# Kernel optimization log

Hardware: AMD Instinct MI355X
Metric: run time of the kernel (lower is better)

The kernel has to match this reference:

```python
import jax, jax.numpy as jnp
import numpy as np

B, S, DM = 4, 2048, 1024
H, D, R = 16, 64, 8

def setup_inputs() -> dict:
    key = jax.random.key(0)
    ks = jax.random.split(key, 32)
    def rn(k, shape, scale=0.02):
        return jax.random.normal(k, shape, dtype=jnp.float32) * scale
    inp = {
        'queries': jax.random.normal(ks[0], (B, S, DM), dtype=jnp.float32),
        'keys':    jax.random.normal(ks[1], (B, S, DM), dtype=jnp.float32),
        'values':  jax.random.normal(ks[2], (B, S, DM), dtype=jnp.float32),
        # base projections, stored [in, out]
        'Wq_w': rn(ks[3], (DM, H * D)), 'Wq_b': jnp.zeros((H * D,), jnp.float32),
        'Wk_w': rn(ks[4], (DM, H * D)), 'Wk_b': jnp.zeros((H * D,), jnp.float32),
        'Wv_w': rn(ks[5], (DM, H * D)), 'Wv_b': jnp.zeros((H * D,), jnp.float32),
        # LoRA adapters (A: in->rank, B: rank->out), Linear layers so both have biases
        'Aq_w': rn(ks[6], (DM, R)), 'Aq_b': jnp.zeros((R,), jnp.float32),
        'Bq_w': rn(ks[7], (R, H * D)), 'Bq_b': jnp.zeros((H * D,), jnp.float32),
        'Ak_w': rn(ks[8], (DM, R)), 'Ak_b': jnp.zeros((R,), jnp.float32),
        'Bk_w': rn(ks[9], (R, H * D)), 'Bk_b': jnp.zeros((H * D,), jnp.float32),
        'Av_w': rn(ks[10], (DM, R)), 'Av_b': jnp.zeros((R,), jnp.float32),
        'Bv_w': rn(ks[11], (R, H * D)), 'Bv_b': jnp.zeros((H * D,), jnp.float32),
        # output merge
        'Wo_w': rn(ks[12], (H * D, DM)), 'Wo_b': jnp.zeros((DM,), jnp.float32),
    }
    return inp


def _attn(queries, keys, values, Wq_w, Wq_b, Wk_w, Wk_b, Wv_w, Wv_b,
          Aq_w, Aq_b, Bq_w, Bq_b, Ak_w, Ak_b, Bk_w, Bk_b, Av_w, Av_b, Bv_w, Bv_b,
          Wo_w, Wo_b):
    b, s, _ = queries.shape
    # QKV projections fused with LoRA low-rank additions
    q = queries @ Wq_w + Wq_b + ((queries @ Aq_w + Aq_b) @ Bq_w + Bq_b)
    k = keys    @ Wk_w + Wk_b + ((keys    @ Ak_w + Ak_b) @ Bk_w + Bk_b)
    # NOTE: source applies the V LoRA adapter to `keys` (self.Av(keys)) - replicated
    v = values  @ Wv_w + Wv_b + ((keys    @ Av_w + Av_b) @ Bv_w + Bv_b)
    q = q.reshape(b, s, H, D).transpose(0, 2, 1, 3)  # [B,H,S,D]
    k = k.reshape(b, s, H, D).transpose(0, 2, 1, 3)
    v = v.reshape(b, s, H, D).transpose(0, 2, 1, 3)
    att = jnp.einsum('bhqd,bhkd->bhqk', q, k)        # [B,H,Sq,Sk]
    causal = jnp.tril(jnp.ones((s, s), dtype=bool))
    att = jnp.where(causal, att, -jnp.inf)
    # NOTE: source softmaxes over dim=2 (query axis) and scales AFTER softmax
    att = jax.nn.softmax(att, axis=2) / jnp.sqrt(jnp.asarray(D, att.dtype))
    out = jnp.einsum('bhqk,bhkd->bhqd', att, v)      # [B,H,S,D]
    out = out.transpose(0, 2, 1, 3).reshape(b, s, H * D)
    return out @ Wo_w + Wo_b


def reference(queries, keys, values, Wq_w, Wq_b, Wk_w, Wk_b, Wv_w, Wv_b,
              Aq_w, Aq_b, Bq_w, Bq_b, Ak_w, Ak_b, Bk_w, Bk_b, Av_w, Av_b, Bv_w, Bv_b,
              Wo_w, Wo_b):
    return _attn(queries, keys, values, Wq_w, Wq_b, Wk_w, Wk_b, Wv_w, Wv_b,
                 Aq_w, Aq_b, Bq_w, Bq_b, Ak_w, Ak_b, Bk_w, Bk_b, Av_w, Av_b, Bv_w, Bv_b,
                 Wo_w, Wo_b)
```

## Files before the change

### kernel.cpp

```cpp
#include <hip/hip_runtime.h>
#include <math.h>
#include <stdint.h>

typedef __bf16 bf16;
typedef __bf16 bf16x8 __attribute__((ext_vector_type(8)));
typedef __bf16 bf16x4 __attribute__((ext_vector_type(4)));
typedef float  floatx4 __attribute__((ext_vector_type(4)));

#define MFMA16(a, b, c) __builtin_amdgcn_mfma_f32_16x16x32_bf16(a, b, c, 0, 0, 0)
#define EXP2(x) __builtin_amdgcn_exp2f(x)

static constexpr int S  = 2048;
static constexpr int DM = 1024;
static constexpr int Dh = 64;
#define NEGBIG (-1e30f)
#define LOG2E  1.44269504088896340736f

__device__ __forceinline__ void gload16(const void* g, void* l) {
  __builtin_amdgcn_global_load_lds(
      (const __attribute__((address_space(1))) void*)(uintptr_t)g,
      (__attribute__((address_space(3))) void*)(uintptr_t)l,
      16, 0, 0);
}

__device__ __forceinline__ int swz(int row, int g) {
  return row * 64 + ((g ^ (row & 7)) << 3);
}

__global__ __launch_bounds__(256) void prep_convert(
    const float* __restrict__ q, const float* __restrict__ k,
    const float* __restrict__ v, bf16* __restrict__ X)
{
  int s = blockIdx.x;
  int c = threadIdx.x * 4;
  size_t src = (size_t)s * DM + c;
  float4 qv = *(const float4*)(q + src);
  float4 vv = *(const float4*)(v + src);
  float4 kv = *(const float4*)(k + src);
  size_t dst = (size_t)s * (3 * DM);
  bf16x4 t;
  t[0] = (bf16)qv.x; t[1] = (bf16)qv.y; t[2] = (bf16)qv.z; t[3] = (bf16)qv.w;
  *(bf16x4*)(X + dst + c) = t;
  t[0] = (bf16)vv.x; t[1] = (bf16)vv.y; t[2] = (bf16)vv.z; t[3] = (bf16)vv.w;
  *(bf16x4*)(X + dst + DM + c) = t;
  t[0] = (bf16)kv.x; t[1] = (bf16)kv.y; t[2] = (bf16)kv.z; t[3] = (bf16)kv.w;
  *(bf16x4*)(X + dst + 2 * DM + c) = t;
}

__global__ __launch_bounds__(256) void fold_weights(
    const float* __restrict__ Wq, const float* __restrict__ Aq, const float* __restrict__ Bq,
    const float* __restrict__ Wk, const float* __restrict__ Ak, const float* __restrict__ Bk,
    const float* __restrict__ Wv, const float* __restrict__ Av, const float* __restrict__ Bv,
    const float* __restrict__ Wo,
    bf16* __restrict__ WqT, bf16* __restrict__ WkT,
    bf16* __restrict__ WvT, bf16* __restrict__ WoT)
{
  __shared__ float tile[32][33];
  const int tx = threadIdx.x, ty = threadIdx.y;
  const int n0 = blockIdx.x * 32, k0 = blockIdx.y * 32;
  for (int mi = 0; mi < 5; ++mi) {
    #pragma unroll
    for (int i = 0; i < 4; ++i) {
      int k = k0 + ty + i * 8, n = n0 + tx;
      float val = 0.f;
      if (mi == 0) {
        val = Wq[(size_t)k * DM + n];
        #pragma unroll
        for (int r = 0; r < 8; ++r) val += Aq[k * 8 + r] * Bq[(size_t)r * DM + n];
      } else if (mi == 1) {
        val = Wk[(size_t)k * DM + n];
        #pragma unroll
        for (int r = 0; r < 8; ++r) val += Ak[k * 8 + r] * Bk[(size_t)r * DM + n];
      } else if (mi == 2) {
        val = Wv[(size_t)k * DM + n];
      } else if (mi == 3) {
        #pragma unroll
        for (int r = 0; r < 8; ++r) val += Av[k * 8 + r] * Bv[(size_t)r * DM + n];
      } else {
        val = Wo[(size_t)k * DM + n];
      }
      tile[ty + i * 8][tx] = val;
    }
    __syncthreads();
    #pragma unroll
    for (int i = 0; i < 4; ++i) {
      int n = n0 + ty + i * 8, k = k0 + tx;
      float val = tile[tx][ty + i * 8];
      if (mi == 0)      WqT[(size_t)n * DM + k] = (bf16)val;
      else if (mi == 1) WkT[(size_t)n * DM + k] = (bf16)val;
      else if (mi == 2) WvT[(size_t)n * 2048 + k] = (bf16)val;
      else if (mi == 3) WvT[(size_t)n * 2048 + 1024 + k] = (bf16)val;
      else              WoT[(size_t)n * DM + k] = (bf16)val;
    }
    __syncthreads();
  }
}

__global__ __launch_bounds__(256) void fold_bias(
    const float* __restrict__ Wqb, const float* __restrict__ Aqb,
    const float* __restrict__ BqW, const float* __restrict__ Bqb,
    const float* __restrict__ Wkb, const float* __restrict__ Akb,
    const float* __restrict__ BkW, const float* __restrict__ Bkb,
    const float* __restrict__ Wvb, const float* __restrict__ Avb,
    const float* __restrict__ BvW, const float* __restrict__ Bvb,
    const float* __restrict__ Wob,
    float* __restrict__ bq, float* __restrict__ bk,
    float* __restrict__ bv, float* __restrict__ bo)
{
  int n = blockIdx.x * 256 + threadIdx.x;
  float aq = Wqb[n] + Bqb[n];
  float ak = Wkb[n] + Bkb[n];
  float av = Wvb[n] + Bvb[n];
  #pragma unroll
  for (int r = 0; r < 8; ++r) {
    aq += Aqb[r] * BqW[(size_t)r * DM + n];
    ak += Akb[r] * BkW[(size_t)r * DM + n];
    av += Avb[r] * BvW[(size_t)r * DM + n];
  }
  bq[n] = aq; bk[n] = ak; bv[n] = av; bo[n] = Wob[n];
}

__global__ __launch_bounds__(256) void gemm_bf16(
    const bf16* __restrict__ A, int lda,
    const bf16* __restrict__ BT, int ldb,
    const float* __restrict__ bias,
    int M, int N, int K, float oscale,
    float* __restrict__ outF, bf16* __restrict__ outB, int mode)
{
  __shared__ bf16 sA[128 * 32];
  __shared__ bf16 sB[128 * 32];
  const int tid = threadIdx.x;
  const int bm0 = blockIdx.y * 128, bn0 = blockIdx.x * 128;
  const int w = tid >> 6, lane = tid & 63, lrow = lane & 15, quad = lane >> 4;
  const int wm = (w >> 1) * 64, wn = (w & 1) * 64;

  const int srow = lane >> 2;
  const int scol = (lane & 3) * 8;
  const bf16* Ag0 = A  + (size_t)(bm0 + w * 32 + srow) * lda + scol;
  const bf16* Ag1 = A  + (size_t)(bm0 + w * 32 + 16 + srow) * lda + scol;
  const bf16* Bg0 = BT + (size_t)(bn0 + w * 32 + srow) * ldb + scol;
  const bf16* Bg1 = BT + (size_t)(bn0 + w * 32 + 16 + srow) * ldb + scol;
  bf16* sA0 = &sA[(w * 32) * 32];
  bf16* sA1 = &sA[(w * 32 + 16) * 32];
  bf16* sB0 = &sB[(w * 32) * 32];
  bf16* sB1 = &sB[(w * 32 + 16) * 32];

  floatx4 zero = {0.f, 0.f, 0.f, 0.f};
  floatx4 acc[4][4];
  #pragma unroll
  for (int i = 0; i < 4; ++i)
    #pragma unroll
    for (int j = 0; j < 4; ++j) acc[i][j] = zero;

  for (int kt = 0; kt < K; kt += 32) {
    __syncthreads();
    gload16(Ag0 + kt, sA0);
    gload16(Ag1 + kt, sA1);
    gload16(Bg0 + kt, sB0);
    gload16(Bg1 + kt, sB1);
    __syncthreads();
    bf16x8 aF[4], bF[4];
    #pragma unroll
    for (int i = 0; i < 4; ++i)
      aF[i] = *(const bf16x8*)&sA[(wm + i * 16 + lrow) * 32 + quad * 8];
    #pragma unroll
    for (int j = 0; j < 4; ++j)
      bF[j] = *(const bf16x8*)&sB[(wn + j * 16 + lrow) * 32 + quad * 8];
    #pragma unroll
    for (int i = 0; i < 4; ++i)
      #pragma unroll
      for (int j = 0; j < 4; ++j)
        acc[i][j] = MFMA16(aF[i], bF[j], acc[i][j]);
  }

  if (mode == 3) {
    #pragma unroll
    for (int i = 0; i < 4; ++i) {
      #pragma unroll
      for (int r = 0; r < 4; ++r) {
        int gm = bm0 + wm + i * 16 + quad * 4 + r;
        float bvr = bias[gm];
        int h = gm >> 6, d = gm & 63;
        #pragma unroll
        for (int j = 0; j < 4; ++j) {
          int gn = bn0 + wn + j * 16 + lrow;
          int b = gn >> 11, s = gn & 2047;
          outB[((size_t)(b * 16 + h) * 64 + d) * 2048 + s] =
              (bf16)(acc[i][j][r] + bvr);
        }
      }
    }
    return;
  }

  float bvs[4];
  #pragma unroll
  for (int j = 0; j < 4; ++j) bvs[j] = bias[bn0 + wn + j * 16 + lrow];

  #pragma unroll
  for (int i = 0; i < 4; ++i) {
    #pragma unroll
    for (int j = 0; j < 4; ++j) {
      #pragma unroll
      for (int r = 0; r < 4; ++r) {
        int gm = bm0 + wm + i * 16 + quad * 4 + r;
        int gn = bn0 + wn + j * 16 + lrow;
        float v = (acc[i][j][r] + bvs[j]) * oscale;
        if (mode == 0) {
          outF[(size_t)gm * N + gn] = v;
        } else {
          int b = gm >> 11, s = gm & 2047, h = gn >> 6, d = gn & 63;
          outB[((size_t)(b * 16 + h) * 2048 + s) * 64 + d] = (bf16)v;
        }
      }
    }
  }
}

__global__ __launch_bounds__(256) void attn_pass1(
    const bf16* __restrict__ Qb, const bf16* __restrict__ Kb,
    float* __restrict__ statC)
{
  const int bh = blockIdx.y;
  const int x = blockIdx.x;
  const int q0a = x * 64, q0b = (31 - x) * 64;
  const int tid = threadIdx.x;
  const int w = tid >> 6, lane = tid & 63, lrow = lane & 15, quad = lane >> 4;
  const bf16* Qh = Qb + (size_t)bh * S * Dh;
  const bf16* Kh = Kb + (size_t)bh * S * Dh;

  int cbase[8];
  #pragma unroll
  for (int cf = 0; cf < 8; ++cf)
    cbase[cf] = (cf < 4) ? (q0a + cf * 16) : (q0b + (cf - 4) * 16);

  bf16x8 kf[8][2];
  #pragma unroll
  for (int cf = 0; cf < 8; ++cf) {
    const bf16* kp = Kh + (size_t)(cbase[cf] + lrow) * Dh + quad * 8;
    kf[cf][0] = *(const bf16x8*)kp;
    kf[cf][1] = *(const bf16x8*)(kp + 32);
  }

  float rm[8], rs[8];
  #pragma unroll
  for (int cf = 0; cf < 8; ++cf) { rm[cf] = NEGBIG; rs[cf] = 0.f; }

  const int qs = q0a + w * 16;
  const bf16* qp0 = Qh + (size_t)(qs + lrow) * Dh + quad * 8;
  bf16x8 a0 = *(const bf16x8*)qp0, a1 = *(const bf16x8*)(qp0 + 32);

  for (int q0 = qs; q0 < S; q0 += 64) {
    bf16x8 n0 = a0, n1 = a1;
    if (q0 + 64 < S) {
      const bf16* np = Qh + (size_t)(q0 + 64 + lrow) * Dh + quad * 8;
      n0 = *(const bf16x8*)np; n1 = *(const bf16x8*)(np + 32);
    }
    #pragma unroll
    for (int cf = 0; cf < 8; ++cf) {
      const int c0f = cbase[cf];
      if (c0f > q0 + 15) continue;
      floatx4 sacc = {0.f, 0.f, 0.f, 0.f};
      sacc = MFMA16(a0, kf[cf][0], sacc);
      sacc = MFMA16(a1, kf[cf][1], sacc);
      float v0 = sacc[0], v1 = sacc[1], v2 = sacc[2], v3 = sacc[3];
      if (q0 < c0f + 15) {
        int c = c0f + lrow, qb = q0 + quad * 4;
        v0 = (qb + 0 >= c) ? v0 : NEGBIG;
        v1 = (qb + 1 >= c) ? v1 : NEGBIG;
        v2 = (qb + 2 >= c) ? v2 : NEGBIG;
        v3 = (qb + 3 >= c) ? v3 : NEGBIG;
      }
      float mt = fmaxf(fmaxf(v0, v1), fmaxf(v2, v3));
      float nm = fmaxf(rm[cf], mt);
      rs[cf] = rs[cf] * EXP2(rm[cf] - nm)
             + EXP2(v0 - nm) + EXP2(v1 - nm)
             + EXP2(v2 - nm) + EXP2(v3 - nm);
      rm[cf] = nm;
    }
    a0 = n0; a1 = n1;
  }

  #pragma unroll
  for (int cf = 0; cf < 8; ++cf) {
    #pragma unroll
    for (int off = 16; off < 64; off <<= 1) {
      float om = __shfl_xor(rm[cf], off, 64);
      float os = __shfl_xor(rs[cf], off, 64);
      float nm = fmaxf(rm[cf], om);
      rs[cf] = rs[cf] * EXP2(rm[cf] - nm) + os * EXP2(om - nm);
      rm[cf] = nm;
    }
  }

  __shared__ float smm[4][128];
  __shared__ float sms[4][128];
  if (quad == 0) {
    #pragma unroll
    for (int cf = 0; cf < 8; ++cf) {
      smm[w][cf * 16 + lrow] = rm[cf];
      sms[w][cf * 16 + lrow] = rs[cf];
    }
  }
  __syncthreads();
  if (tid < 128) {
    float m = smm[0][tid], sum = sms[0][tid];
    #pragma unroll
    for (int ww = 1; ww < 4; ++ww) {
      float om = smm[ww][tid], os = sms[ww][tid];
      float nm = fmaxf(m, om);
      sum = sum * EXP2(m - nm) + os * EXP2(om - nm);
      m = nm;
    }
    int col = (tid < 64) ? (q0a + tid) : (q0b + tid - 64);
    statC[(size_t)bh * S + col] = m + 3.0f + __log2f(sum);
  }
}

__global__ __launch_bounds__(256) void attn_pass2(
    const bf16* __restrict__ Qb, const bf16* __restrict__ Kb,
    const bf16* __restrict__ Vt, const float* __restrict__ statC,
    bf16* __restrict__ AttOut)
{
  const int bh = blockIdx.y;
  const int x = blockIdx.x;
  const int q0a = x * 64, q0b = (31 - x) * 64;
  const int tid = threadIdx.x;
  const int w = tid >> 6, lane = tid & 63, lrow = lane & 15, quad = lane >> 4;
  const bf16* Qh = Qb + (size_t)bh * S * Dh;
  const bf16* Kh = Kb + (size_t)bh * S * Dh;
  const bf16* Vh = Vt + (size_t)bh * Dh * S;
  const float* sth = statC + (size_t)bh * S;

  __shared__ bf16 sK[64 * 64];
  __shared__ bf16 sV[64 * 64];
  __shared__ bf16 pbuf[4][32 * 64];

  const int r0m[2] = { q0a + w * 16, q0b + w * 16 };
  bf16x8 qf[2][2];
  #pragma unroll
  for (int mi = 0; mi < 2; ++mi) {
    const bf16* qp = Qh + (size_t)(r0m[mi] + lrow) * Dh + quad * 8;
    qf[mi][0] = *(const bf16x8*)qp;
    qf[mi][1] = *(const bf16x8*)(qp + 32);
  }

  floatx4 zero = {0.f, 0.f, 0.f, 0.f};
  floatx4 accO[2][4];
  #pragma unroll
  for (int mi = 0; mi < 2; ++mi)
    #pragma unroll
    for (int nf = 0; nf < 4; ++nf) accO[mi][nf] = zero;

  const int sr = tid >> 3;
  const int g  = tid & 7;
  const int nT = 32 - x;
  bf16* const pw = &pbuf[w][0];

  bf16x8 kg0 = *(const bf16x8*)(Kh + (size_t)sr * Dh + g * 8);
  bf16x8 kg1 = *(const bf16x8*)(Kh + (size_t)(sr + 32) * Dh + g * 8);
  bf16x8 vg0 = *(const bf16x8*)(Vh + (size_t)sr * S + g * 8);
  bf16x8 vg1 = *(const bf16x8*)(Vh + (size_t)(sr + 32) * S + g * 8);

  for (int kt = 0; kt < nT; ++kt) {
    const int kc = kt * 64;
    __syncthreads();
    *(bf16x8*)&sK[swz(sr, g)]      = kg0;
    *(bf16x8*)&sK[swz(sr + 32, g)] = kg1;
    *(bf16x8*)&sV[swz(sr, g)]      = vg0;
    *(bf16x8*)&sV[swz(sr + 32, g)] = vg1;
    float4 c4[4];
    #pragma unroll
    for (int cf = 0; cf < 4; ++cf)
      c4[cf] = *(const float4*)&sth[kc + cf * 16 + quad * 4];
    __syncthreads();
    if (kt + 1 < nT) {
      const int kn = kc + 64;
      kg0 = *(const bf16x8*)(Kh + (size_t)(kn + sr) * Dh + g * 8);
      kg1 = *(const bf16x8*)(Kh + (size_t)(kn + sr + 32) * Dh + g * 8);
      vg0 = *(const bf16x8*)(Vh + (size_t)sr * S + kn + g * 8);
      vg1 = *(const bf16x8*)(Vh + (size_t)(sr + 32) * S + kn + g * 8);
    }

    bool actH[2][2];
    #pragma unroll
    for (int mi = 0; mi < 2; ++mi) {
      actH[mi][0] = kc      <= r0m[mi] + 15;
      actH[mi][1] = kc + 32 <= r0m[mi] + 15;
    }

    #pragma unroll
    for (int cf = 0; cf < 4; ++cf) {
      const int hh = cf >> 1;
      if (!actH[0][hh] && !actH[1][hh]) continue;
      const int c0f = kc + cf * 16;
      const int cl = cf * 16;
      bf16x8 kf0 = *(const bf16x8*)&sK[swz(cl + lrow, quad)];
      bf16x8 kf1 = *(const bf16x8*)&sK[swz(cl + lrow, 4 + quad)];
      const float* cc = &c4[cf].x;
      const int crb = c0f + quad * 4;
      #pragma unroll
      for (int mi = 0; mi < 2; ++mi) {
        if (!actH[mi][hh]) continue;
        const int r0 = r0m[mi];
        const int gq = cf * 2 + (quad >> 1);
        const int poff = (mi * 16 + lrow) * 64 +
                         ((gq ^ (lrow & 7)) << 3) + (quad & 1) * 4;
        bf16x4 pk;
        if (c0f > r0 + 15) {
          pk[0] = pk[1] = pk[2] = pk[3] = (bf16)0.f;
        } else {
          floatx4 sacc = zero;
          sacc = MFMA16(kf0, qf[mi][0], sacc);
          sacc = MFMA16(kf1, qf[mi][1], sacc);
          const bool fullf = (c0f + 15 <= r0);
          const int qlane = r0 + lrow;
          #pragma unroll
          for (int r = 0; r < 4; ++r) {
            float p = EXP2(sacc[r] - cc[r]);
            if (!fullf) p = (crb + r <= qlane) ? p : 0.f;
            pk[r] = (bf16)p;
          }
        }
        *(bf16x4*)(pw + poff) = pk;
      }
    }

    #pragma unroll
    for (int hh = 0; hh < 2; ++hh) {
      if (!actH[0][hh] && !actH[1][hh]) continue;
      bf16x8 vf[4];
      #pragma unroll
      for (int nf = 0; nf < 4; ++nf)
        vf[nf] = *(const bf16x8*)&sV[swz(nf * 16 + lrow, hh * 4 + quad)];
      #pragma unroll
      for (int mi = 0; mi < 2; ++mi) {
        if (!actH[mi][hh]) continue;
        bf16x8 pf = *(const bf16x8*)(pw + swz(mi * 16 + lrow, hh * 4 + quad));
        #pragma unroll
        for (int nf = 0; nf < 4; ++nf)
          accO[mi][nf] = MFMA16(pf, vf[nf], accO[mi][nf]);
      }
    }
  }

  const int b = bh >> 4, h = bh & 15;
  #pragma unroll
  for (int mi = 0; mi < 2; ++mi) {
    #pragma unroll
    for (int nf = 0; nf < 4; ++nf) {
      #pragma unroll
      for (int r = 0; r < 4; ++r) {
        int qq = r0m[mi] + quad * 4 + r;
        int d = nf * 16 + lrow;
        AttOut[((size_t)(b * S + qq)) * DM + h * 64 + d] = (bf16)accO[mi][nf][r];
      }
    }
  }
}

extern "C" void kernel_launch(void* const* d_in, const int* in_sizes, int n_in,
                              void* d_out, int out_size, void* d_ws, size_t ws_size,
                              hipStream_t stream) {
  (void)in_sizes; (void)n_in; (void)out_size; (void)ws_size;
  const float* queries = (const float*)d_in[0];
  const float* keys    = (const float*)d_in[1];
  const float* values  = (const float*)d_in[2];
  const float* Wq_w = (const float*)d_in[3];  const float* Wq_b = (const float*)d_in[4];
  const float* Wk_w = (const float*)d_in[5];  const float* Wk_b = (const float*)d_in[6];
  const float* Wv_w = (const float*)d_in[7];  const float* Wv_b = (const float*)d_in[8];
  const float* Aq_w = (const float*)d_in[9];  const float* Aq_b = (const float*)d_in[10];
  const float* Bq_w = (const float*)d_in[11]; const float* Bq_b = (const float*)d_in[12];
  const float* Ak_w = (const float*)d_in[13]; const float* Ak_b = (const float*)d_in[14];
  const float* Bk_w = (const float*)d_in[15]; const float* Bk_b = (const float*)d_in[16];
  const float* Av_w = (const float*)d_in[17]; const float* Av_b = (const float*)d_in[18];
  const float* Bv_w = (const float*)d_in[19]; const float* Bv_b = (const float*)d_in[20];
  const float* Wo_w = (const float*)d_in[21]; const float* Wo_b = (const float*)d_in[22];
  float* out = (float*)d_out;

  char* ws = (char*)d_ws;
  size_t off = 0;
  auto alloc = [&](size_t bytes) -> void* {
    void* p = ws + off;
    off += (bytes + 255) & ~(size_t)255;
    return p;
  };
  bf16*  X_all  = (bf16*)alloc((size_t)8192 * 3072 * 2);
  bf16*  Qb     = (bf16*)alloc((size_t)64 * 2048 * 64 * 2);
  bf16*  Kb     = (bf16*)alloc((size_t)64 * 2048 * 64 * 2);
  bf16*  Vt     = (bf16*)alloc((size_t)64 * 64 * 2048 * 2);
  bf16*  AttOut = (bf16*)alloc((size_t)8192 * 1024 * 2);
  bf16*  WqT    = (bf16*)alloc((size_t)1024 * 1024 * 2);
  bf16*  WkT    = (bf16*)alloc((size_t)1024 * 1024 * 2);
  bf16*  WvT    = (bf16*)alloc((size_t)1024 * 2048 * 2);
  bf16*  WoT    = (bf16*)alloc((size_t)1024 * 1024 * 2);
  float* bq     = (float*)alloc(1024 * 4);
  float* bk     = (float*)alloc(1024 * 4);
  float* bv     = (float*)alloc(1024 * 4);
  float* bo     = (float*)alloc(1024 * 4);
  float* statC  = (float*)alloc((size_t)64 * 2048 * 4);

  prep_convert<<<8192, 256, 0, stream>>>(queries, keys, values, X_all);
  fold_weights<<<dim3(32, 32), dim3(32, 8), 0, stream>>>(
      Wq_w, Aq_w, Bq_w, Wk_w, Ak_w, Bk_w, Wv_w, Av_w, Bv_w, Wo_w,
      WqT, WkT, WvT, WoT);
  fold_bias<<<4, 256, 0, stream>>>(
      Wq_b, Aq_b, Bq_w, Bq_b, Wk_b, Ak_b, Bk_w, Bk_b,
      Wv_b, Av_b, Bv_w, Bv_b, Wo_b, bq, bk, bv, bo);

  gemm_bf16<<<dim3(8, 64), 256, 0, stream>>>(X_all,        3072, WqT, 1024, bq, 8192, 1024, 1024, LOG2E, nullptr, Qb, 1);
  gemm_bf16<<<dim3(8, 64), 256, 0, stream>>>(X_all + 2048, 3072, WkT, 1024, bk, 8192, 1024, 1024, 1.0f,  nullptr, Kb, 1);
  gemm_bf16<<<dim3(64, 8), 256, 0, stream>>>(WvT, 2048, X_all + 1024, 3072, bv, 1024, 8192, 2048, 1.0f, nullptr, Vt, 3);

  attn_pass1<<<dim3(16, 64), 256, 0, stream>>>(Qb, Kb, statC);
  attn_pass2<<<dim3(16, 64), 256, 0, stream>>>(Qb, Kb, Vt, statC, AttOut);

  gemm_bf16<<<dim3(8, 64), 256, 0, stream>>>(AttOut, 1024, WoT, 1024, bo, 8192, 1024, 1024, 1.0f, out, nullptr, 0);
}
```

Measured before the change: 471.5 us.

## Double-buffer swizzled GEMM tiles and split attention pass2 across eight waves

The bf16 GEMM moves to 512 threads per block with 8 waves, each owning a 32x64 sub-tile. It double-buffers the A/B LDS tiles with a single barrier per k-step, prefetching the next tile while the current one feeds the MFMAs, and adds an XOR swizzle on LDS columns to reduce bank conflicts. attn_pass2 also moves to 512 threads, so each wave handles one 16-row query strip instead of two, which halves per-wave accumulators and P buffers. The aims are to hide global-load latency and raise occupancy. The cost is more barrier participants per block and reliance on the async LDS loads having completed at the barrier.

```diff
diff --git a/kernel.cpp b/kernel.cpp
--- a/kernel.cpp
+++ b/kernel.cpp
@@ -120,54 +120,63 @@
   bq[n] = aq; bk[n] = ak; bv[n] = av; bo[n] = Wob[n];
 }
 
-__global__ __launch_bounds__(256) void gemm_bf16(
+__global__ __launch_bounds__(512, 4) void gemm_bf16(
     const bf16* __restrict__ A, int lda,
     const bf16* __restrict__ BT, int ldb,
     const float* __restrict__ bias,
     int M, int N, int K, float oscale,
     float* __restrict__ outF, bf16* __restrict__ outB, int mode)
 {
-  __shared__ bf16 sA[128 * 32];
-  __shared__ bf16 sB[128 * 32];
+  __shared__ bf16 sA[2][128 * 32];
+  __shared__ bf16 sB[2][128 * 32];
   const int tid = threadIdx.x;
   const int bm0 = blockIdx.y * 128, bn0 = blockIdx.x * 128;
   const int w = tid >> 6, lane = tid & 63, lrow = lane & 15, quad = lane >> 4;
-  const int wm = (w >> 1) * 64, wn = (w & 1) * 64;
-
-  const int srow = lane >> 2;
-  const int scol = (lane & 3) * 8;
-  const bf16* Ag0 = A  + (size_t)(bm0 + w * 32 + srow) * lda + scol;
-  const bf16* Ag1 = A  + (size_t)(bm0 + w * 32 + 16 + srow) * lda + scol;
-  const bf16* Bg0 = BT + (size_t)(bn0 + w * 32 + srow) * ldb + scol;
-  const bf16* Bg1 = BT + (size_t)(bn0 + w * 32 + 16 + srow) * ldb + scol;
-  bf16* sA0 = &sA[(w * 32) * 32];
-  bf16* sA1 = &sA[(w * 32 + 16) * 32];
-  bf16* sB0 = &sB[(w * 32) * 32];
-  bf16* sB1 = &sB[(w * 32 + 16) * 32];
+  const int wm = (w >> 1) * 32, wn = (w & 1) * 64;
+
+  const int srow = tid >> 2;
+  const int sg   = (tid & 3) ^ ((srow >> 1) & 3);
+  const bf16* Ag = A  + (size_t)(bm0 + srow) * lda + sg * 8;
+  const bf16* Bg = BT + (size_t)(bn0 + srow) * ldb + sg * 8;
+  const int wb = w * 512;
+
+  int aoff[2], boff[4];
+  #pragma unroll
+  for (int i = 0; i < 2; ++i) {
+    int r = wm + i * 16 + lrow;
+    aoff[i] = r * 32 + ((quad ^ ((r >> 1) & 3)) << 3);
+  }
+  #pragma unroll
+  for (int j = 0; j < 4; ++j) {
+    int r = wn + j * 16 + lrow;
+    boff[j] = r * 32 + ((quad ^ ((r >> 1) & 3)) << 3);
+  }
 
   floatx4 zero = {0.f, 0.f, 0.f, 0.f};
-  floatx4 acc[4][4];
-  #pragma unroll
-  for (int i = 0; i < 4; ++i)
+  floatx4 acc[2][4];
+  #pragma unroll
+  for (int i = 0; i < 2; ++i)
     #pragma unroll
     for (int j = 0; j < 4; ++j) acc[i][j] = zero;
 
-  for (int kt = 0; kt < K; kt += 32) {
+  const int nk = K >> 5;
+  gload16(Ag, &sA[0][wb]);
+  gload16(Bg, &sB[0][wb]);
+
+  for (int t = 0; t < nk; ++t) {
+    const int cur = t & 1;
     __syncthreads();
-    gload16(Ag0 + kt, sA0);
-    gload16(Ag1 + kt, sA1);
-    gload16(Bg0 + kt, sB0);
-    gload16(Bg1 + kt, sB1);
-    __syncthreads();
-    bf16x8 aF[4], bF[4];
-    #pragma unroll
-    for (int i = 0; i < 4; ++i)
-      aF[i] = *(const bf16x8*)&sA[(wm + i * 16 + lrow) * 32 + quad * 8];
-    #pragma unroll
-    for (int j = 0; j < 4; ++j)
-      bF[j] = *(const bf16x8*)&sB[(wn + j * 16 + lrow) * 32 + quad * 8];
-    #pragma unroll
-    for (int i = 0; i < 4; ++i)
+    if (t + 1 < nk) {
+      gload16(Ag + (size_t)(t + 1) * 32, &sA[cur ^ 1][wb]);
+      gload16(Bg + (size_t)(t + 1) * 32, &sB[cur ^ 1][wb]);
+    }
+    bf16x8 aF[2], bF[4];
+    #pragma unroll
+    for (int i = 0; i < 2; ++i) aF[i] = *(const bf16x8*)&sA[cur][aoff[i]];
+    #pragma unroll
+    for (int j = 0; j < 4; ++j) bF[j] = *(const bf16x8*)&sB[cur][boff[j]];
+    #pragma unroll
+    for (int i = 0; i < 2; ++i)
       #pragma unroll
       for (int j = 0; j < 4; ++j)
         acc[i][j] = MFMA16(aF[i], bF[j], acc[i][j]);
@@ -175,7 +184,7 @@
 
   if (mode == 3) {
     #pragma unroll
-    for (int i = 0; i < 4; ++i) {
+    for (int i = 0; i < 2; ++i) {
       #pragma unroll
       for (int r = 0; r < 4; ++r) {
         int gm = bm0 + wm + i * 16 + quad * 4 + r;
@@ -198,7 +207,7 @@
   for (int j = 0; j < 4; ++j) bvs[j] = bias[bn0 + wn + j * 16 + lrow];
 
   #pragma unroll
-  for (int i = 0; i < 4; ++i) {
+  for (int i = 0; i < 2; ++i) {
     #pragma unroll
     for (int j = 0; j < 4; ++j) {
       #pragma unroll
@@ -317,7 +326,7 @@
   }
 }
 
-__global__ __launch_bounds__(256) void attn_pass2(
+__global__ __launch_bounds__(512, 8) void attn_pass2(
     const bf16* __restrict__ Qb, const bf16* __restrict__ Kb,
     const bf16* __restrict__ Vt, const float* __restrict__ statC,
     bf16* __restrict__ AttOut)
@@ -327,6 +336,8 @@
   const int q0a = x * 64, q0b = (31 - x) * 64;
   const int tid = threadIdx.x;
   const int w = tid >> 6, lane = tid & 63, lrow = lane & 15, quad = lane >> 4;
+  const int mi = w >> 2;
+  const int r0 = (mi ? q0b : q0a) + (w & 3) * 16;
   const bf16* Qh = Qb + (size_t)bh * S * Dh;
   const bf16* Kh = Kb + (size_t)bh * S * Dh;
   const bf16* Vh = Vt + (size_t)bh * Dh * S;
@@ -334,127 +345,98 @@
 
   __shared__ bf16 sK[64 * 64];
   __shared__ bf16 sV[64 * 64];
-  __shared__ bf16 pbuf[4][32 * 64];
-
-  const int r0m[2] = { q0a + w * 16, q0b + w * 16 };
-  bf16x8 qf[2][2];
-  #pragma unroll
-  for (int mi = 0; mi < 2; ++mi) {
-    const bf16* qp = Qh + (size_t)(r0m[mi] + lrow) * Dh + quad * 8;
-    qf[mi][0] = *(const bf16x8*)qp;
-    qf[mi][1] = *(const bf16x8*)(qp + 32);
-  }
+  __shared__ bf16 pbuf[8][16 * 64];
+
+  const bf16* qp = Qh + (size_t)(r0 + lrow) * Dh + quad * 8;
+  bf16x8 qf0 = *(const bf16x8*)qp;
+  bf16x8 qf1 = *(const bf16x8*)(qp + 32);
 
   floatx4 zero = {0.f, 0.f, 0.f, 0.f};
-  floatx4 accO[2][4];
-  #pragma unroll
-  for (int mi = 0; mi < 2; ++mi)
-    #pragma unroll
-    for (int nf = 0; nf < 4; ++nf) accO[mi][nf] = zero;
+  floatx4 accO[4];
+  #pragma unroll
+  for (int nf = 0; nf < 4; ++nf) accO[nf] = zero;
 
   const int sr = tid >> 3;
   const int g  = tid & 7;
   const int nT = 32 - x;
   bf16* const pw = &pbuf[w][0];
 
-  bf16x8 kg0 = *(const bf16x8*)(Kh + (size_t)sr * Dh + g * 8);
-  bf16x8 kg1 = *(const bf16x8*)(Kh + (size_t)(sr + 32) * Dh + g * 8);
-  bf16x8 vg0 = *(const bf16x8*)(Vh + (size_t)sr * S + g * 8);
-  bf16x8 vg1 = *(const bf16x8*)(Vh + (size_t)(sr + 32) * S + g * 8);
+  bf16x8 kg = *(const bf16x8*)(Kh + (size_t)sr * Dh + g * 8);
+  bf16x8 vg = *(const bf16x8*)(Vh + (size_t)sr * S + g * 8);
 
   for (int kt = 0; kt < nT; ++kt) {
     const int kc = kt * 64;
     __syncthreads();
-    *(bf16x8*)&sK[swz(sr, g)]      = kg0;
-    *(bf16x8*)&sK[swz(sr + 32, g)] = kg1;
-    *(bf16x8*)&sV[swz(sr, g)]      = vg0;
-    *(bf16x8*)&sV[swz(sr + 32, g)] = vg1;
+    *(bf16x8*)&sK[swz(sr, g)] = kg;
+    *(bf16x8*)&sV[swz(sr, g)] = vg;
+    __syncthreads();
     float4 c4[4];
     #pragma unroll
     for (int cf = 0; cf < 4; ++cf)
       c4[cf] = *(const float4*)&sth[kc + cf * 16 + quad * 4];
-    __syncthreads();
     if (kt + 1 < nT) {
       const int kn = kc + 64;
-      kg0 = *(const bf16x8*)(Kh + (size_t)(kn + sr) * Dh + g * 8);
-      kg1 = *(const bf16x8*)(Kh + (size_t)(kn + sr + 32) * Dh + g * 8);
-      vg0 = *(const bf16x8*)(Vh + (size_t)sr * S + kn + g * 8);
-      vg1 = *(const bf16x8*)(Vh + (size_t)(sr + 32) * S + kn + g * 8);
-    }
-
-    bool actH[2][2];
-    #pragma unroll
-    for (int mi = 0; mi < 2; ++mi) {
-      actH[mi][0] = kc      <= r0m[mi] + 15;
-      actH[mi][1] = kc + 32 <= r0m[mi] + 15;
-    }
+      kg = *(const bf16x8*)(Kh + (size_t)(kn + sr) * Dh + g * 8);
+      vg = *(const bf16x8*)(Vh + (size_t)sr * S + kn + g * 8);
+    }
+
+    const bool act0 = kc      <= r0 + 15;
+    const bool act1 = kc + 32 <= r0 + 15;
 
     #pragma unroll
     for (int cf = 0; cf < 4; ++cf) {
-      const int hh = cf >> 1;
-      if (!actH[0][hh] && !actH[1][hh]) continue;
+      const bool acth = (cf >> 1) ? act1 : act0;
+      if (!acth) continue;
       const int c0f = kc + cf * 16;
       const int cl = cf * 16;
-      bf16x8 kf0 = *(const bf16x8*)&sK[swz(cl + lrow, quad)];
-      bf16x8 kf1 = *(const bf16x8*)&sK[swz(cl + lrow, 4 + quad)];
-      const float* cc = &c4[cf].x;
-      const int crb = c0f + quad * 4;
-      #pragma unroll
-      for (int mi = 0; mi < 2; ++mi) {
-        if (!actH[mi][hh]) continue;
-        const int r0 = r0m[mi];
-        const int gq = cf * 2 + (quad >> 1);
-        const int poff = (mi * 16 + lrow) * 64 +
-                         ((gq ^ (lrow & 7)) << 3) + (quad & 1) * 4;
-        bf16x4 pk;
-        if (c0f > r0 + 15) {
-          pk[0] = pk[1] = pk[2] = pk[3] = (bf16)0.f;
-        } else {
-          floatx4 sacc = zero;
-          sacc = MFMA16(kf0, qf[mi][0], sacc);
-          sacc = MFMA16(kf1, qf[mi][1], sacc);
-          const bool fullf = (c0f + 15 <= r0);
-          const int qlane = r0 + lrow;
-          #pragma unroll
-          for (int r = 0; r < 4; ++r) {
-            float p = EXP2(sacc[r] - cc[r]);
-            if (!fullf) p = (crb + r <= qlane) ? p : 0.f;
-            pk[r] = (bf16)p;
-          }
+      const int gq = cf * 2 + (quad >> 1);
+      const int poff = lrow * 64 + ((gq ^ (lrow & 7)) << 3) + (quad & 1) * 4;
+      bf16x4 pk;
+      if (c0f > r0 + 15) {
+        pk[0] = pk[1] = pk[2] = pk[3] = (bf16)0.f;
+      } else {
+        bf16x8 kf0 = *(const bf16x8*)&sK[swz(cl + lrow, quad)];
+        bf16x8 kf1 = *(const bf16x8*)&sK[swz(cl + lrow, 4 + quad)];
+        floatx4 sacc = zero;
+        sacc = MFMA16(kf0, qf0, sacc);
+        sacc = MFMA16(kf1, qf1, sacc);
+        const float* cc = &c4[cf].x;
+        const int crb = c0f + quad * 4;
+        const bool fullf = (c0f + 15 <= r0);
+        const int qlane = r0 + lrow;
+        #pragma unroll
+        for (int r = 0; r < 4; ++r) {
+          float p = EXP2(sacc[r] - cc[r]);
+          if (!fullf) p = (crb + r <= qlane) ? p : 0.f;
+          pk[r] = (bf16)p;
         }
-        *(bf16x4*)(pw + poff) = pk;
       }
+      *(bf16x4*)(pw + poff) = pk;
     }
 
     #pragma unroll
     for (int hh = 0; hh < 2; ++hh) {
-      if (!actH[0][hh] && !actH[1][hh]) continue;
+      const bool acth = hh ? act1 : act0;
+      if (!acth) continue;
       bf16x8 vf[4];
       #pragma unroll
       for (int nf = 0; nf < 4; ++nf)
         vf[nf] = *(const bf16x8*)&sV[swz(nf * 16 + lrow, hh * 4 + quad)];
+      bf16x8 pf = *(const bf16x8*)(pw + swz(lrow, hh * 4 + quad));
       #pragma unroll
-      for (int mi = 0; mi < 2; ++mi) {
-        if (!actH[mi][hh]) continue;
-        bf16x8 pf = *(const bf16x8*)(pw + swz(mi * 16 + lrow, hh * 4 + quad));
-        #pragma unroll
-        for (int nf = 0; nf < 4; ++nf)
-          accO[mi][nf] = MFMA16(pf, vf[nf], accO[mi][nf]);
-      }
+      for (int nf = 0; nf < 4; ++nf)
+        accO[nf] = MFMA16(pf, vf[nf], accO[nf]);
     }
   }
 
   const int b = bh >> 4, h = bh & 15;
   #pragma unroll
-  for (int mi = 0; mi < 2; ++mi) {
-    #pragma unroll
-    for (int nf = 0; nf < 4; ++nf) {
-      #pragma unroll
-      for (int r = 0; r < 4; ++r) {
-        int qq = r0m[mi] + quad * 4 + r;
-        int d = nf * 16 + lrow;
-        AttOut[((size_t)(b * S + qq)) * DM + h * 64 + d] = (bf16)accO[mi][nf][r];
-      }
+  for (int nf = 0; nf < 4; ++nf) {
+    #pragma unroll
+    for (int r = 0; r < 4; ++r) {
+      int qq = r0 + quad * 4 + r;
+      int d = nf * 16 + lrow;
+      AttOut[((size_t)(b * S + qq)) * DM + h * 64 + d] = (bf16)accO[nf][r];
     }
   }
 }
@@ -508,12 +490,12 @@
       Wq_b, Aq_b, Bq_w, Bq_b, Wk_b, Ak_b, Bk_w, Bk_b,
       Wv_b, Av_b, Bv_w, Bv_b, Wo_b, bq, bk, bv, bo);
 
-  gemm_bf16<<<dim3(8, 64), 256, 0, stream>>>(X_all,        3072, WqT, 1024, bq, 8192, 1024, 1024, LOG2E, nullptr, Qb, 1);
-  gemm_bf16<<<dim3(8, 64), 256, 0, stream>>>(X_all + 2048, 3072, WkT, 1024, bk, 8192, 1024, 1024, 1.0f,  nullptr, Kb, 1);
-  gemm_bf16<<<dim3(64, 8), 256, 0, stream>>>(WvT, 2048, X_all + 1024, 3072, bv, 1024, 8192, 2048, 1.0f, nullptr, Vt, 3);
+  gemm_bf16<<<dim3(8, 64), 512, 0, stream>>>(X_all,        3072, WqT, 1024, bq, 8192, 1024, 1024, LOG2E, nullptr, Qb, 1);
+  gemm_bf16<<<dim3(8, 64), 512, 0, stream>>>(X_all + 2048, 3072, WkT, 1024, bk, 8192, 1024, 1024, 1.0f,  nullptr, Kb, 1);
+  gemm_bf16<<<dim3(64, 8), 512, 0, stream>>>(WvT, 2048, X_all + 1024, 3072, bv, 1024, 8192, 2048, 1.0f, nullptr, Vt, 3);
 
   attn_pass1<<<dim3(16, 64), 256, 0, stream>>>(Qb, Kb, statC);
-  attn_pass2<<<dim3(16, 64), 256, 0, stream>>>(Qb, Kb, Vt, statC, AttOut);
-
-  gemm_bf16<<<dim3(8, 64), 256, 0, stream>>>(AttOut, 1024, WoT, 1024, bo, 8192, 1024, 1024, 1.0f, out, nullptr, 0);
-}
+  attn_pass2<<<dim3(16, 64), 512, 0, stream>>>(Qb, Kb, Vt, statC, AttOut);
+
+  gemm_bf16<<<dim3(8, 64), 512, 0, stream>>>(AttOut, 1024, WoT, 1024, bo, 8192, 1024, 1024, 1.0f, out, nullptr, 0);
+}
```

New measurement: 654.5 us. +38.8%, slower.

## Double-buffer GEMM LDS tiles, swizzle layout, and use 8 waves per block

Applied to the files above, without the earlier changes.

The bf16 GEMM now double-buffers its A/B LDS tiles, so the next k-slice is prefetched with global_load_lds while MFMAs run on the current one, and only one barrier is needed per iteration. The LDS layout is XOR-swizzled to reduce bank conflicts on fragment reads. Blocks grow to 512 threads (8 waves), each wave owning a 32x64 sub-tile, which halves accumulator registers per thread and raises latency hiding. The cost is double the LDS per block. Correctness also depends on the single barrier ordering the prefetch against reads of the other buffer.

```diff
diff --git a/kernel.cpp b/kernel.cpp
--- a/kernel.cpp
+++ b/kernel.cpp
@@ -120,54 +120,63 @@
   bq[n] = aq; bk[n] = ak; bv[n] = av; bo[n] = Wob[n];
 }
 
-__global__ __launch_bounds__(256) void gemm_bf16(
+__global__ __launch_bounds__(512, 4) void gemm_bf16(
     const bf16* __restrict__ A, int lda,
     const bf16* __restrict__ BT, int ldb,
     const float* __restrict__ bias,
     int M, int N, int K, float oscale,
     float* __restrict__ outF, bf16* __restrict__ outB, int mode)
 {
-  __shared__ bf16 sA[128 * 32];
-  __shared__ bf16 sB[128 * 32];
+  __shared__ bf16 sA[2][128 * 32];
+  __shared__ bf16 sB[2][128 * 32];
   const int tid = threadIdx.x;
   const int bm0 = blockIdx.y * 128, bn0 = blockIdx.x * 128;
   const int w = tid >> 6, lane = tid & 63, lrow = lane & 15, quad = lane >> 4;
-  const int wm = (w >> 1) * 64, wn = (w & 1) * 64;
-
-  const int srow = lane >> 2;
-  const int scol = (lane & 3) * 8;
-  const bf16* Ag0 = A  + (size_t)(bm0 + w * 32 + srow) * lda + scol;
-  const bf16* Ag1 = A  + (size_t)(bm0 + w * 32 + 16 + srow) * lda + scol;
-  const bf16* Bg0 = BT + (size_t)(bn0 + w * 32 + srow) * ldb + scol;
-  const bf16* Bg1 = BT + (size_t)(bn0 + w * 32 + 16 + srow) * ldb + scol;
-  bf16* sA0 = &sA[(w * 32) * 32];
-  bf16* sA1 = &sA[(w * 32 + 16) * 32];
-  bf16* sB0 = &sB[(w * 32) * 32];
-  bf16* sB1 = &sB[(w * 32 + 16) * 32];
+  const int wm = (w >> 1) * 32, wn = (w & 1) * 64;
+
+  const int srow = tid >> 2;
+  const int sg   = (tid & 3) ^ ((srow >> 1) & 3);
+  const bf16* Ag = A  + (size_t)(bm0 + srow) * lda + sg * 8;
+  const bf16* Bg = BT + (size_t)(bn0 + srow) * ldb + sg * 8;
+  const int wb = w * 512;
+
+  int aoff[2], boff[4];
+  #pragma unroll
+  for (int i = 0; i < 2; ++i) {
+    int r = wm + i * 16 + lrow;
+    aoff[i] = r * 32 + ((quad ^ ((r >> 1) & 3)) << 3);
+  }
+  #pragma unroll
+  for (int j = 0; j < 4; ++j) {
+    int r = wn + j * 16 + lrow;
+    boff[j] = r * 32 + ((quad ^ ((r >> 1) & 3)) << 3);
+  }
 
   floatx4 zero = {0.f, 0.f, 0.f, 0.f};
-  floatx4 acc[4][4];
-  #pragma unroll
-  for (int i = 0; i < 4; ++i)
+  floatx4 acc[2][4];
+  #pragma unroll
+  for (int i = 0; i < 2; ++i)
     #pragma unroll
     for (int j = 0; j < 4; ++j) acc[i][j] = zero;
 
-  for (int kt = 0; kt < K; kt += 32) {
+  const int nk = K >> 5;
+  gload16(Ag, &sA[0][wb]);
+  gload16(Bg, &sB[0][wb]);
+
+  for (int t = 0; t < nk; ++t) {
+    const int cur = t & 1;
     __syncthreads();
-    gload16(Ag0 + kt, sA0);
-    gload16(Ag1 + kt, sA1);
-    gload16(Bg0 + kt, sB0);
-    gload16(Bg1 + kt, sB1);
-    __syncthreads();
-    bf16x8 aF[4], bF[4];
-    #pragma unroll
-    for (int i = 0; i < 4; ++i)
-      aF[i] = *(const bf16x8*)&sA[(wm + i * 16 + lrow) * 32 + quad * 8];
-    #pragma unroll
-    for (int j = 0; j < 4; ++j)
-      bF[j] = *(const bf16x8*)&sB[(wn + j * 16 + lrow) * 32 + quad * 8];
-    #pragma unroll
-    for (int i = 0; i < 4; ++i)
+    if (t + 1 < nk) {
+      gload16(Ag + (size_t)(t + 1) * 32, &sA[cur ^ 1][wb]);
+      gload16(Bg + (size_t)(t + 1) * 32, &sB[cur ^ 1][wb]);
+    }
+    bf16x8 aF[2], bF[4];
+    #pragma unroll
+    for (int i = 0; i < 2; ++i) aF[i] = *(const bf16x8*)&sA[cur][aoff[i]];
+    #pragma unroll
+    for (int j = 0; j < 4; ++j) bF[j] = *(const bf16x8*)&sB[cur][boff[j]];
+    #pragma unroll
+    for (int i = 0; i < 2; ++i)
       #pragma unroll
       for (int j = 0; j < 4; ++j)
         acc[i][j] = MFMA16(aF[i], bF[j], acc[i][j]);
@@ -175,7 +184,7 @@
 
   if (mode == 3) {
     #pragma unroll
-    for (int i = 0; i < 4; ++i) {
+    for (int i = 0; i < 2; ++i) {
       #pragma unroll
       for (int r = 0; r < 4; ++r) {
         int gm = bm0 + wm + i * 16 + quad * 4 + r;
@@ -198,7 +207,7 @@
   for (int j = 0; j < 4; ++j) bvs[j] = bias[bn0 + wn + j * 16 + lrow];
 
   #pragma unroll
-  for (int i = 0; i < 4; ++i) {
+  for (int i = 0; i < 2; ++i) {
     #pragma unroll
     for (int j = 0; j < 4; ++j) {
       #pragma unroll
@@ -508,12 +517,12 @@
       Wq_b, Aq_b, Bq_w, Bq_b, Wk_b, Ak_b, Bk_w, Bk_b,
       Wv_b, Av_b, Bv_w, Bv_b, Wo_b, bq, bk, bv, bo);
 
-  gemm_bf16<<<dim3(8, 64), 256, 0, stream>>>(X_all,        3072, WqT, 1024, bq, 8192, 1024, 1024, LOG2E, nullptr, Qb, 1);
-  gemm_bf16<<<dim3(8, 64), 256, 0, stream>>>(X_all + 2048, 3072, WkT, 1024, bk, 8192, 1024, 1024, 1.0f,  nullptr, Kb, 1);
-  gemm_bf16<<<dim3(64, 8), 256, 0, stream>>>(WvT, 2048, X_all + 1024, 3072, bv, 1024, 8192, 2048, 1.0f, nullptr, Vt, 3);
+  gemm_bf16<<<dim3(8, 64), 512, 0, stream>>>(X_all,        3072, WqT, 1024, bq, 8192, 1024, 1024, LOG2E, nullptr, Qb, 1);
+  gemm_bf16<<<dim3(8, 64), 512, 0, stream>>>(X_all + 2048, 3072, WkT, 1024, bk, 8192, 1024, 1024, 1.0f,  nullptr, Kb, 1);
+  gemm_bf16<<<dim3(64, 8), 512, 0, stream>>>(WvT, 2048, X_all + 1024, 3072, bv, 1024, 8192, 2048, 1.0f, nullptr, Vt, 3);
 
   attn_pass1<<<dim3(16, 64), 256, 0, stream>>>(Qb, Kb, statC);
   attn_pass2<<<dim3(16, 64), 256, 0, stream>>>(Qb, Kb, Vt, statC, AttOut);
 
-  gemm_bf16<<<dim3(8, 64), 256, 0, stream>>>(AttOut, 1024, WoT, 1024, bo, 8192, 1024, 1024, 1.0f, out, nullptr, 0);
-}
+  gemm_bf16<<<dim3(8, 64), 512, 0, stream>>>(AttOut, 1024, WoT, 1024, bo, 8192, 1024, 1024, 1.0f, out, nullptr, 0);
+}
```

Result: faster. 444.2 us (-5.8%).
